# Performance work log

Hardware: AMD Instinct MI355X
Metric: run time of the kernel (lower is better)

The kernel has to match this reference:

```python
import jax, jax.numpy as jnp
import numpy as np

# Action space: 3 discrete action types, 8 options each (MultiDiscrete nvec)
ACTION_NUMS = np.array([8, 8, 8])
A_TOTAL = int(ACTION_NUMS.sum())          # 24
START_IDX = np.cumsum([0, *ACTION_NUMS[:-1]])  # [0, 8, 16]
F, N, D = 4096, 64, 256                   # frames, agents(actions per frame), feat_size
HID = 140                                 # fixed in ForwardNet


def setup_inputs() -> dict:
    key = jax.random.key(0)
    ks = jax.random.split(key, 8)
    s = lambda fan_in: 1.0 / np.sqrt(fan_in)
    return {
        "current_feature": jax.random.normal(ks[0], (F, N, D), jnp.float32),
        "next_feature": jax.random.normal(ks[1], (F, N, D), jnp.float32),
        "actions": jax.random.randint(ks[2], (F, 3, N), 0, 8, dtype=jnp.int32),
        "W1": jax.random.normal(ks[3], (D + A_TOTAL, HID), jnp.float32) * s(D + A_TOTAL),
        "b1": jnp.zeros((HID,), jnp.float32),
        "W2": jax.random.normal(ks[4], (HID, D), jnp.float32) * s(HID),
        "b2": jnp.zeros((D,), jnp.float32),
        "Wi": jax.random.normal(ks[5], (2 * D, A_TOTAL), jnp.float32) * s(2 * D),
        "bi": jnp.zeros((A_TOTAL,), jnp.float32),
    }


def actions2onehot(actions):
    # actions: [F, T, N] int. Vectorized replacement for the triple Python loop:
    # each (frame, agent) row gets a 1 at START_IDX[type] + action, per type.
    start = jnp.asarray(START_IDX, actions.dtype)          # [T]
    idx = actions + start[None, :, None]                    # [F, T, N]
    oh = jax.nn.one_hot(idx, A_TOTAL, dtype=jnp.float32)    # [F, T, N, A]
    return oh.sum(axis=1)                                   # [F, N, A] (column ranges disjoint)


def reference(current_feature, next_feature, actions, W1, b1, W2, b2, Wi, bi):
    action_one_hot = actions2onehot(actions)                       # [F, N, 24]
    # Forward dynamics (attn_target != ICM branch)
    fwd_in = jnp.concatenate([current_feature, action_one_hot], axis=2)  # [F, N, 280]
    h = jax.nn.leaky_relu(fwd_in @ W1 + b1, negative_slope=0.1)
    next_feature_pred = h @ W2 + b2                                # [F, N, 256]
    # Inverse dynamics
    inv_in = jnp.concatenate([current_feature, next_feature], axis=2)   # [F, N, 512]
    action_pred = inv_in @ Wi + bi                                 # [F, N, 24] per-type logits concatenated
    return next_feature_pred, action_pred
```

## Files before the change

### kernel.cpp

```cpp
#include <hip/hip_runtime.h>
#include <hip/hip_bf16.h>
#include <stdint.h>


typedef __attribute__((ext_vector_type(8))) short short8;
typedef __attribute__((ext_vector_type(4))) float float4v;

#define MFMA16 __builtin_amdgcn_mfma_f32_16x16x32_bf16

__device__ __align__(16) uint16_t g_wpack[98816];

static __device__ __forceinline__ void gl_lds16(const void* g, void* l) {
    __builtin_amdgcn_global_load_lds(
        (const __attribute__((address_space(1))) unsigned int*)g,
        (__attribute__((address_space(3))) unsigned int*)l, 16, 0, 0);
}

static __device__ __forceinline__ uint16_t f2bf(float f) {
    __hip_bfloat16 h = __float2bfloat16(f);
    return *reinterpret_cast<uint16_t*>(&h);
}

static __device__ __forceinline__ int pk2(float lo, float hi) {
    __hip_bfloat162 b = __float22bfloat162_rn(make_float2(lo, hi));
    int u; __builtin_memcpy(&u, &b, 4); return u;
}

static __device__ __forceinline__ short8 cvt8(float4v x0, float4v x1) {
    union { __hip_bfloat162 b2[4]; short8 s; } u;
    u.b2[0] = __float22bfloat162_rn(make_float2(x0[0], x0[1]));
    u.b2[1] = __float22bfloat162_rn(make_float2(x0[2], x0[3]));
    u.b2[2] = __float22bfloat162_rn(make_float2(x1[0], x1[1]));
    u.b2[3] = __float22bfloat162_rn(make_float2(x1[2], x1[3]));
    return u.s;
}

__global__ __launch_bounds__(256) void pack_weights(
    const float* __restrict__ W1, const float* __restrict__ W2,
    const float* __restrict__ Wi)
{
    int e = blockIdx.x * 256 + threadIdx.x;
    if (e >= 98816) return;
    if (e >= 41472 && e < 82432) {
        int le = e - 41472;
        int i = le & 7, lane = (le >> 3) & 63, frag = le >> 9;
        int kt = frag >> 4, nt = frag & 15;
        int k = kt * 32 + ((i >= 4) ? 16 : 0) + ((lane >> 4) << 2) + (i & 3);
        int n = nt * 16 + (lane & 15);
        float v = (k < 140) ? W2[k * 256 + n] : 0.0f;
        g_wpack[e] = f2bf(v);
        return;
    }
    const float* W; int NT, Kr, Nr, ld, le, base;
    if (e < 41472) { W = W1; NT = 9; Kr = 280; Nr = 140; ld = 140; le = e;         base = 0; }
    else           { W = Wi; NT = 2; Kr = 512; Nr = 24;  ld = 24;  le = e - 82432; base = 82432; }
    int i = le & 7, lane = (le >> 3) & 63, frag = le >> 9;
    int kt = frag / NT, nt = frag - kt * NT;
    int k = kt * 32 + ((lane >> 4) << 3) + i;
    int n = nt * 16 + (lane & 15);
    float v = (k < Kr && n < Nr) ? W[k * ld + n] : 0.0f;
    g_wpack[base + le] = f2bf(v);
}

__global__ __launch_bounds__(512, 4) void icm_main(
    const float* __restrict__ cf, const float* __restrict__ nf,
    const int* __restrict__ act,
    const float* __restrict__ b1, const float* __restrict__ b2,
    const float* __restrict__ bi,
    float* __restrict__ out)
{
    __shared__ __align__(16) char smem[65536];
    char* bufA = smem;
    char* bufB = smem + 32768;

    const int tid  = threadIdx.x;
    const int wave = tid >> 6;
    const int lane = tid & 63;
    const int lhi  = lane >> 4;
    const int llo  = lane & 15;

    const long rowbase = (long)blockIdx.x * 128 + wave * 16;
    const char* gw = (const char*)g_wpack;
    const float4v fz = {0.f, 0.f, 0.f, 0.f};

    auto stage_slot = [&](char* dst, int kt) {
        const char* w1b = gw + kt * 9216;
        const char* wlo = gw + 164864 + kt * 2048;
        const char* whi = gw + 181248 + kt * 2048;
        #pragma unroll
        for (int k = 0; k < 2; ++k) {
            int b = k * 8192 + wave * 1024;
            if (b < 13312) {
                const char* src = (b < 9216) ? (w1b + b)
                                : (b < 11264) ? (wlo + (b - 9216))
                                              : (whi + (b - 11264));
                gl_lds16(src + lane * 16, dst + b);
            }
        }
    };
    auto stage8 = [&](char* dst, const char* src) {
        int b = wave * 1024;
        gl_lds16(src + b + lane * 16, dst + b);
    };

    int i0, i1, i2;
    {
        long r = rowbase + llo;
        long f = r >> 6; int n = (int)(r & 63);
        i0 = act[(f * 3 + 0) * 64 + n];
        i1 = act[(f * 3 + 1) * 64 + n] + 8;
        i2 = act[(f * 3 + 2) * 64 + n] + 16;
    }

    float4v acc1[9];
    float4v acc3[2];
    #pragma unroll
    for (int n = 0; n < 9; ++n) acc1[n] = fz;
    acc3[0] = fz; acc3[1] = fz;

    const float* cfb = cf + (rowbase + llo) * 256 + lhi * 8;
    const float* nfb = nf + (rowbase + llo) * 256 + lhi * 8;

    float4v pa0, pa1, pb0, pb1;
    float4v qa0, qa1, qb0, qb1;

    auto g1m = [&](const char* base, int kt) {
        short8 ac = (kt & 1) ? cvt8(pb0, pb1) : cvt8(pa0, pa1);
        short8 an = (kt & 1) ? cvt8(qb0, qb1) : cvt8(qa0, qa1);
        if (kt <= 5) {
            int o = (kt + 2) * 32;
            if (kt & 1) {
                pb0 = *(const float4v*)(cfb + o); pb1 = *(const float4v*)(cfb + o + 4);
                qb0 = *(const float4v*)(nfb + o); qb1 = *(const float4v*)(nfb + o + 4);
            } else {
                pa0 = *(const float4v*)(cfb + o); pa1 = *(const float4v*)(cfb + o + 4);
                qa0 = *(const float4v*)(nfb + o); qa1 = *(const float4v*)(nfb + o + 4);
            }
        }
        #pragma unroll
        for (int nt = 0; nt < 9; ++nt) {
            short8 bf = *(const short8*)(base + (nt << 10) + (lane << 4));
            acc1[nt] = MFMA16(bf, ac, acc1[nt], 0, 0, 0);
        }
        #pragma unroll
        for (int nt = 0; nt < 2; ++nt) {
            short8 bf = *(const short8*)(base + 9216 + (nt << 10) + (lane << 4));
            acc3[nt] = MFMA16(bf, ac, acc3[nt], 0, 0, 0);
        }
        #pragma unroll
        for (int nt = 0; nt < 2; ++nt) {
            short8 bf = *(const short8*)(base + 11264 + (nt << 10) + (lane << 4));
            acc3[nt] = MFMA16(bf, an, acc3[nt], 0, 0, 0);
        }
    };

    stage_slot(bufA, 0); stage_slot(bufA + 13312, 1);
    pa0 = *(const float4v*)(cfb);      pa1 = *(const float4v*)(cfb + 4);
    pb0 = *(const float4v*)(cfb + 32); pb1 = *(const float4v*)(cfb + 36);
    qa0 = *(const float4v*)(nfb);      qa1 = *(const float4v*)(nfb + 4);
    qb0 = *(const float4v*)(nfb + 32); qb1 = *(const float4v*)(nfb + 36);
    __syncthreads();

    stage_slot(bufB, 2); stage_slot(bufB + 13312, 3);
    g1m(bufA, 0); g1m(bufA + 13312, 1);
    __syncthreads();

    stage_slot(bufA, 4); stage_slot(bufA + 13312, 5);
    g1m(bufB, 2); g1m(bufB + 13312, 3);
    __syncthreads();

    stage_slot(bufB, 6); stage_slot(bufB + 13312, 7);
    g1m(bufA, 4); g1m(bufA + 13312, 5);
    __syncthreads();

    stage_slot(bufA, 8);
    g1m(bufB, 6); g1m(bufB + 13312, 7);
    __syncthreads();

    stage8(bufB, gw + 82944);
    stage8(bufB + 8192, gw + 82944 + 16384);
    {
        short8 a;
        #pragma unroll
        for (int i = 0; i < 8; ++i) {
            int kk = lhi * 8 + i;
            a[i] = (kk == i0 || kk == i1 || kk == i2) ? (short)0x3F80 : (short)0;
        }
        #pragma unroll
        for (int nt = 0; nt < 9; ++nt) {
            short8 bf = *(const short8*)(bufA + (nt << 10) + (lane << 4));
            acc1[nt] = MFMA16(bf, a, acc1[nt], 0, 0, 0);
        }
    }
    float* out2 = out + 67108864L;
    #pragma unroll
    for (int nt = 0; nt < 2; ++nt) {
        if (nt == 0 || lhi < 2) {
            float4v biv = *(const float4v*)(bi + nt * 16 + lhi * 4);
            long row = rowbase + llo;
            float4v v = acc3[nt];
            v[0] += biv[0]; v[1] += biv[1]; v[2] += biv[2]; v[3] += biv[3];
            *(float4v*)(out2 + row * 24 + nt * 16 + lhi * 4) = v;
        }
    }
    short8 hb[5];
    #pragma unroll
    for (int kt = 0; kt < 5; ++kt) {
        int cLo = 2 * kt * 16 + lhi * 4;
        int cHi = (2 * kt + 1) * 16 + lhi * 4;
        if (cLo > 136) cLo = 136;
        float4v bLo = *(const float4v*)(b1 + cLo);
        float4v bHi = (kt < 4) ? *(const float4v*)(b1 + cHi) : fz;
        union { int d[4]; short8 s; } t;
        float v0 = acc1[2 * kt][0] + bLo[0]; v0 = v0 > 0.f ? v0 : 0.1f * v0;
        float v1 = acc1[2 * kt][1] + bLo[1]; v1 = v1 > 0.f ? v1 : 0.1f * v1;
        float v2 = acc1[2 * kt][2] + bLo[2]; v2 = v2 > 0.f ? v2 : 0.1f * v2;
        float v3 = acc1[2 * kt][3] + bLo[3]; v3 = v3 > 0.f ? v3 : 0.1f * v3;
        t.d[0] = pk2(v0, v1);
        t.d[1] = pk2(v2, v3);
        if (kt < 4) {
            float w0 = acc1[2 * kt + 1][0] + bHi[0]; w0 = w0 > 0.f ? w0 : 0.1f * w0;
            float w1 = acc1[2 * kt + 1][1] + bHi[1]; w1 = w1 > 0.f ? w1 : 0.1f * w1;
            float w2 = acc1[2 * kt + 1][2] + bHi[2]; w2 = w2 > 0.f ? w2 : 0.1f * w2;
            float w3 = acc1[2 * kt + 1][3] + bHi[3]; w3 = w3 > 0.f ? w3 : 0.1f * w3;
            t.d[2] = pk2(w0, w1);
            t.d[3] = pk2(w2, w3);
        } else { t.d[2] = 0; t.d[3] = 0; }
        hb[kt] = t.s;
    }
    __syncthreads();

    auto g2 = [&](const char* wb, int kt, float4v* acc2) {
        #pragma unroll
        for (int n = 0; n < 8; ++n) {
            short8 bf = *(const short8*)(wb + (n << 10) + (lane << 4));
            acc2[n] = MFMA16(bf, hb[kt], acc2[n], 0, 0, 0);
        }
    };
    auto store_p = [&](int p, float4v* acc2) {
        #pragma unroll
        for (int n = 0; n < 8; ++n) {
            int nt = p * 8 + n;
            float4v b2v = *(const float4v*)(b2 + nt * 16 + lhi * 4);
            long row = rowbase + llo;
            float4v v = acc2[n];
            v[0] += b2v[0]; v[1] += b2v[1]; v[2] += b2v[2]; v[3] += b2v[3];
            *(float4v*)(out + row * 256 + nt * 16 + lhi * 4) = v;
        }
    };
    const char* w2t = gw + 82944;

    {
        float4v acc2[8];
        #pragma unroll
        for (int n = 0; n < 8; ++n) acc2[n] = fz;

        stage8(bufA, w2t + 2 * 16384);
        stage8(bufA + 8192, w2t + 3 * 16384);
        g2(bufB, 0, acc2); g2(bufB + 8192, 1, acc2);
        __syncthreads();

        stage8(bufB, w2t + 4 * 16384);
        stage8(bufB + 8192, w2t + 8192);
        g2(bufA, 2, acc2); g2(bufA + 8192, 3, acc2);
        __syncthreads();

        stage8(bufA, w2t + 16384 + 8192);
        stage8(bufA + 8192, w2t + 2 * 16384 + 8192);
        g2(bufB, 4, acc2);
        store_p(0, acc2);
        __syncthreads();
    }
    {
        float4v acc2[8];
        #pragma unroll
        for (int n = 0; n < 8; ++n) acc2[n] = fz;

        stage8(bufB, w2t + 3 * 16384 + 8192);
        g2(bufB + 8192, 0, acc2);
        g2(bufA, 1, acc2); g2(bufA + 8192, 2, acc2);
        __syncthreads();

        stage8(bufA, w2t + 4 * 16384 + 8192);
        g2(bufB, 3, acc2);
        __syncthreads();

        g2(bufA, 4, acc2);
        store_p(1, acc2);
    }
}

extern "C" void kernel_launch(void* const* d_in, const int* in_sizes, int n_in,
                              void* d_out, int out_size, void* d_ws, size_t ws_size,
                              hipStream_t stream) {
    const float *cf = nullptr, *nf = nullptr, *W1 = nullptr, *b1 = nullptr;
    const float *W2 = nullptr, *b2 = nullptr, *Wi = nullptr, *bi = nullptr;
    const int *ac = nullptr;
    for (int i = 0; i < n_in; ++i) {
        int s = in_sizes[i];
        const void* p = d_in[i];
        switch (s) {
            case 67108864: if (!cf) cf = (const float*)p; else nf = (const float*)p; break;
            case 786432:   ac = (const int*)p;   break;
            case 39200:    W1 = (const float*)p; break;
            case 140:      b1 = (const float*)p; break;
            case 35840:    W2 = (const float*)p; break;
            case 256:      b2 = (const float*)p; break;
            case 12288:    Wi = (const float*)p; break;
            case 24:       bi = (const float*)p; break;
            default: break;
        }
    }
    float* ob = (float*)d_out;

    pack_weights<<<386, 256, 0, stream>>>(W1, W2, Wi);
    icm_main<<<2048, 512, 0, stream>>>(cf, nf, ac, b1, b2, bi, ob);
}
```

Measured before the change: 189.2 us.

## Deepen activation prefetch to four K-tiles ahead and relax occupancy bound

Raises the register-prefetch depth for the current and next feature activations from two K-tiles to four, issuing global loads further ahead of the MFMA steps that consume them. To make room for the extra registers, the launch bounds minimum-blocks hint drops from 4 to 3 per CU. The aim is to hide global memory latency better in this bandwidth-bound kernel, at the cost of possibly lower occupancy.

```diff
diff --git a/kernel.cpp b/kernel.cpp
--- a/kernel.cpp
+++ b/kernel.cpp
@@ -62,7 +62,7 @@
     g_wpack[base + le] = f2bf(v);
 }
 
-__global__ __launch_bounds__(512, 4) void icm_main(
+__global__ __launch_bounds__(512, 3) void icm_main(
     const float* __restrict__ cf, const float* __restrict__ nf,
     const int* __restrict__ act,
     const float* __restrict__ b1, const float* __restrict__ b2,
@@ -121,22 +121,14 @@
     const float* cfb = cf + (rowbase + llo) * 256 + lhi * 8;
     const float* nfb = nf + (rowbase + llo) * 256 + lhi * 8;
 
-    float4v pa0, pa1, pb0, pb1;
-    float4v qa0, qa1, qb0, qb1;
-
-    auto g1m = [&](const char* base, int kt) {
-        short8 ac = (kt & 1) ? cvt8(pb0, pb1) : cvt8(pa0, pa1);
-        short8 an = (kt & 1) ? cvt8(qb0, qb1) : cvt8(qa0, qa1);
-        if (kt <= 5) {
-            int o = (kt + 2) * 32;
-            if (kt & 1) {
-                pb0 = *(const float4v*)(cfb + o); pb1 = *(const float4v*)(cfb + o + 4);
-                qb0 = *(const float4v*)(nfb + o); qb1 = *(const float4v*)(nfb + o + 4);
-            } else {
-                pa0 = *(const float4v*)(cfb + o); pa1 = *(const float4v*)(cfb + o + 4);
-                qa0 = *(const float4v*)(nfb + o); qa1 = *(const float4v*)(nfb + o + 4);
-            }
-        }
+    float4v f0a, f0b, f1a, f1b, f2a, f2b, f3a, f3b;
+    float4v g0a, g0b, g1a, g1b, g2a, g2b, g3a, g3b;
+
+#define LDF(Sa, Sb, P, KT) do { \
+    Sa = *(const float4v*)((P) + (KT) * 32); \
+    Sb = *(const float4v*)((P) + (KT) * 32 + 4); } while (0)
+
+    auto mstep = [&](const char* base, short8 ac, short8 an) {
         #pragma unroll
         for (int nt = 0; nt < 9; ++nt) {
             short8 bf = *(const short8*)(base + (nt << 10) + (lane << 4));
@@ -155,26 +147,46 @@
     };
 
     stage_slot(bufA, 0); stage_slot(bufA + 13312, 1);
-    pa0 = *(const float4v*)(cfb);      pa1 = *(const float4v*)(cfb + 4);
-    pb0 = *(const float4v*)(cfb + 32); pb1 = *(const float4v*)(cfb + 36);
-    qa0 = *(const float4v*)(nfb);      qa1 = *(const float4v*)(nfb + 4);
-    qb0 = *(const float4v*)(nfb + 32); qb1 = *(const float4v*)(nfb + 36);
+    LDF(f0a, f0b, cfb, 0); LDF(f1a, f1b, cfb, 1);
+    LDF(f2a, f2b, cfb, 2); LDF(f3a, f3b, cfb, 3);
+    LDF(g0a, g0b, nfb, 0); LDF(g1a, g1b, nfb, 1);
+    LDF(g2a, g2b, nfb, 2); LDF(g3a, g3b, nfb, 3);
     __syncthreads();
 
     stage_slot(bufB, 2); stage_slot(bufB + 13312, 3);
-    g1m(bufA, 0); g1m(bufA + 13312, 1);
+    {
+        short8 ac = cvt8(f0a, f0b), an = cvt8(g0a, g0b);
+        LDF(f0a, f0b, cfb, 4); LDF(g0a, g0b, nfb, 4);
+        mstep(bufA, ac, an);
+    }
+    {
+        short8 ac = cvt8(f1a, f1b), an = cvt8(g1a, g1b);
+        LDF(f1a, f1b, cfb, 5); LDF(g1a, g1b, nfb, 5);
+        mstep(bufA + 13312, ac, an);
+    }
     __syncthreads();
 
     stage_slot(bufA, 4); stage_slot(bufA + 13312, 5);
-    g1m(bufB, 2); g1m(bufB + 13312, 3);
+    {
+        short8 ac = cvt8(f2a, f2b), an = cvt8(g2a, g2b);
+        LDF(f2a, f2b, cfb, 6); LDF(g2a, g2b, nfb, 6);
+        mstep(bufB, ac, an);
+    }
+    {
+        short8 ac = cvt8(f3a, f3b), an = cvt8(g3a, g3b);
+        LDF(f3a, f3b, cfb, 7); LDF(g3a, g3b, nfb, 7);
+        mstep(bufB + 13312, ac, an);
+    }
     __syncthreads();
 
     stage_slot(bufB, 6); stage_slot(bufB + 13312, 7);
-    g1m(bufA, 4); g1m(bufA + 13312, 5);
+    mstep(bufA,         cvt8(f0a, f0b), cvt8(g0a, g0b));
+    mstep(bufA + 13312, cvt8(f1a, f1b), cvt8(g1a, g1b));
     __syncthreads();
 
     stage_slot(bufA, 8);
-    g1m(bufB, 6); g1m(bufB + 13312, 7);
+    mstep(bufB,         cvt8(f2a, f2b), cvt8(g2a, g2b));
+    mstep(bufB + 13312, cvt8(f3a, f3b), cvt8(g3a, g3b));
     __syncthreads();
 
     stage8(bufB, gw + 82944);
@@ -288,6 +300,7 @@
         g2(bufA, 4, acc2);
         store_p(1, acc2);
     }
+#undef LDF
 }
 
 extern "C" void kernel_launch(void* const* d_in, const int* in_sizes, int n_in,
```

Result: slower. 229.2 us (+21.1%).
